# Optimization experiments

Hardware: AMD Instinct MI355X
Metric: run time of the kernel (lower is better)

Reference implementation:

```python
import jax, jax.numpy as jnp
import numpy as np

B, N, E = 256, 128, 262144
LABEL_DIM, MAX_DEGREE, RW_DIM = 29, 16, 16
F = 128
NUM_LABELS = LABEL_DIM + MAX_DEGREE + RW_DIM  # 61
SK_ITER, SK_TAU = 6, 1.0


def _edges(k):
    k1, k2, k3 = jax.random.split(k, 3)
    g = jax.random.randint(k1, (E,), 0, B)
    src = g * N + jax.random.randint(k2, (E,), 0, N)
    dst = g * N + jax.random.randint(k3, (E,), 0, N)
    return src, dst


def setup_inputs():
    key = jax.random.key(0)
    ks = jax.random.split(key, 20)
    ntot = B * N
    s = 0.05
    nrm = lambda k, shp: jax.random.normal(k, shp, dtype=jnp.float32) * s
    src1, dst1 = _edges(ks[3])
    src2, dst2 = _edges(ks[7])
    return {
        'x1': jax.random.uniform(ks[0], (ntot, LABEL_DIM), dtype=jnp.float32),
        'cent1': jax.random.randint(ks[1], (ntot,), 0, MAX_DEGREE),
        'rw1': jax.random.uniform(ks[2], (ntot, RW_DIM), dtype=jnp.float32),
        'src1': src1, 'dst1': dst1,
        'x2': jax.random.uniform(ks[4], (ntot, LABEL_DIM), dtype=jnp.float32),
        'cent2': jax.random.randint(ks[5], (ntot,), 0, MAX_DEGREE),
        'rw2': jax.random.uniform(ks[6], (ntot, RW_DIM), dtype=jnp.float32),
        'src2': src2, 'dst2': dst2,
        'degree_emb': nrm(ks[8], (MAX_DEGREE, MAX_DEGREE)),
        'init_W': nrm(ks[9], (NUM_LABELS, F)), 'init_b': jnp.zeros((F,), jnp.float32),
        'W1': nrm(ks[10], (F, F)), 'b1': jnp.zeros((F,), jnp.float32),
        'W2': nrm(ks[11], (F, F)), 'b2': jnp.zeros((F,), jnp.float32),
        'W3': nrm(ks[12], (F, F)), 'b3': jnp.zeros((F,), jnp.float32),
        'A_aff': nrm(ks[13], (F, F)) + jnp.eye(F, dtype=jnp.float32),
        'sc_W1': nrm(ks[14], (8 * F, 64)), 'sc_b1': jnp.zeros((64,), jnp.float32),
        'sc_W2': nrm(ks[15], (64, 1)), 'sc_b2': jnp.zeros((1,), jnp.float32),
        'topk': 8,
    }


def gcn_conv(x, W, b, src, dst):
    # GCNConv: x' = D^{-1/2} (A + I) D^{-1/2} x W + b
    n = x.shape[0]
    h = x @ W
    loops = jnp.arange(n)
    s = jnp.concatenate([src, loops])
    d = jnp.concatenate([dst, loops])
    deg = jax.ops.segment_sum(jnp.ones_like(d, dtype=h.dtype), d, n)
    dinv = jax.lax.rsqrt(jnp.maximum(deg, 1.0))
    w = dinv[s] * dinv[d]
    return jax.ops.segment_sum(h[s] * w[:, None], d, n) + b


def conv_pass(feat, src, dst, W1, b1, W2, b2, W3, b3):
    f1 = gcn_conv(feat, W1, b1, src, dst)
    f2 = gcn_conv(jax.nn.relu(f1), W2, b2, src, dst)
    f3 = gcn_conv(jax.nn.relu(f2), W3, b3, src, dst)
    return f1, f2, f3


def affinity(xa, xb, A):
    Xa = xa.reshape(B, N, -1)
    Xb = xb.reshape(B, N, -1)
    return jnp.einsum('bif,fg,bjg->bij', Xa, A, Xb)


def soft_topk(scores, ks_tgt, n_iter, tau):
    # Entropic-OT soft top-k (Xie et al.) over flattened affinity entries vs 2 anchors,
    # normalized by SK_ITER log-domain Sinkhorn iterations.
    b, n, m = scores.shape
    L = n * m
    x = scores.reshape(b, L)
    a_lo = x.min(axis=1, keepdims=True) - 1.0
    a_hi = x.max(axis=1, keepdims=True) + 1.0
    anchors = jnp.concatenate([a_lo, a_hi], axis=1)      # [b, 2]
    logK = -jnp.abs(x[:, :, None] - anchors[:, None, :]) / tau  # [b, L, 2]
    log_mu = jnp.full((b, L), -jnp.log(float(L)), dtype=x.dtype)
    k = ks_tgt[:, None]
    nu = jnp.concatenate([(L - k) / L, k / L], axis=1)   # [b, 2]
    log_nu = jnp.log(nu)

    def body(carry, _):
        f, g = carry
        f = log_mu - jax.nn.logsumexp(logK + g[:, None, :], axis=2)
        g = log_nu - jax.nn.logsumexp(logK + f[:, :, None], axis=1)
        return (f, g), None

    init = (jnp.zeros((b, L), x.dtype), jnp.zeros((b, 2), x.dtype))
    (f, g), _ = jax.lax.scan(body, init, None, length=n_iter)
    gamma = jnp.exp(logK + f[:, :, None] + g[:, None, :])
    prob = (gamma[:, :, 1] * L).reshape(b, n, m)
    return gamma, prob


def reference(x1, cent1, rw1, src1, dst1, x2, cent2, rw2, src2, dst2,
              degree_emb, init_W, init_b, W1, b1, W2, b2, W3, b3, A_aff,
              sc_W1, sc_b1, sc_W2, sc_b2, topk):
    feat1 = jax.nn.relu(jnp.concatenate([x1, degree_emb[cent1], rw1], axis=1) @ init_W + init_b)
    feat2 = jax.nn.relu(jnp.concatenate([x2, degree_emb[cent2], rw2], axis=1) @ init_W + init_b)
    f11, f12, f13 = conv_pass(feat1, src1, dst1, W1, b1, W2, b2, W3, b3)
    f21, f22, f23 = conv_pass(feat2, src2, dst2, W1, b1, W2, b2, W3, b3)

    gt_ks = jnp.full((B,), topk / 2.0, dtype=feat1.dtype)
    _, sim1 = soft_topk(affinity(feat1, feat2, A_aff), gt_ks, SK_ITER, SK_TAU)
    _, sim2 = soft_topk(affinity(f13, f23, A_aff), gt_ks, SK_ITER, SK_TAU)

    gf1 = jnp.concatenate([feat1, f11, f12, f13], axis=1).reshape(B, N, -1).sum(axis=1)   # global_add_pool
    gf2 = jnp.concatenate([feat2, f21, f22, f23], axis=1).reshape(B, N, -1).max(axis=1)   # global_max_pool
    scores = jnp.concatenate([gf1, gf2], axis=1)  # [B, 8F]
    h = jax.nn.relu(scores @ sc_W1 + sc_b1)
    ged = jax.nn.sigmoid((h @ sc_W2 + sc_b2).reshape(-1))
    return ged, sim1, sim2
```

## Files before the change

kernel.cpp:

```cpp
#include <hip/hip_runtime.h>
#include <math.h>

#define BATCH 256
#define NNODE 128
#define NT    32768
#define FDIM  128
#define NEDGE 262144
#define LBL   29
#define MAXDEG 16
#define RWD   16
#define NTF   (NT * FDIM)

__global__ void k_deg2(const int* __restrict__ dst1, const int* __restrict__ dst2,
                       int* __restrict__ d1, int* __restrict__ d2) {
  int e = blockIdx.x * 256 + threadIdx.x;
  if (e < NEDGE) atomicAdd(&d1[dst1[e]], 1);
  else if (e < 2 * NEDGE) atomicAdd(&d2[dst2[e - NEDGE]], 1);
}
__global__ __launch_bounds__(1024) void k_scan2(const int* __restrict__ degi1,
                                                int* __restrict__ ofs1, int* __restrict__ cur1,
                                                float* __restrict__ dinv1,
                                                const int* __restrict__ degi2,
                                                int* __restrict__ ofs2, int* __restrict__ cur2,
                                                float* __restrict__ dinv2) {
  const int* degi = blockIdx.x ? degi2 : degi1;
  int* ofs   = blockIdx.x ? ofs2  : ofs1;
  int* cur   = blockIdx.x ? cur2  : cur1;
  float* dnv = blockIdx.x ? dinv2 : dinv1;
  __shared__ int part[1024];
  int t = threadIdx.x;
  int base = t * 32;
  int loc[32]; int sum = 0;
#pragma unroll
  for (int u = 0; u < 32; ++u) {
    int dg = degi[base + u];
    loc[u] = sum; sum += dg;
    dnv[base + u] = rsqrtf((float)(dg + 1));
  }
  part[t] = sum;
  __syncthreads();
  for (int off = 1; off < 1024; off <<= 1) {
    int v = (t >= off) ? part[t - off] : 0;
    __syncthreads();
    part[t] += v;
    __syncthreads();
  }
  int excl = (t == 0) ? 0 : part[t - 1];
#pragma unroll
  for (int u = 0; u < 32; ++u) {
    int o = excl + loc[u];
    ofs[base + u] = o; cur[base + u] = o;
  }
}
__global__ void k_fill2(const int* __restrict__ src1, const int* __restrict__ dst1,
                        int* __restrict__ cur1, int* __restrict__ csr1,
                        const int* __restrict__ src2, const int* __restrict__ dst2,
                        int* __restrict__ cur2, int* __restrict__ csr2) {
  int e = blockIdx.x * 256 + threadIdx.x;
  if (e < NEDGE) {
    int pos = atomicAdd(&cur1[dst1[e]], 1);
    csr1[pos] = src1[e];
  } else if (e < 2 * NEDGE) {
    e -= NEDGE;
    int pos = atomicAdd(&cur2[dst2[e]], 1);
    csr2[pos] = src2[e];
  }
}

__global__ __launch_bounds__(256, 2) void k_chain(
    const float* __restrict__ x1, const int* __restrict__ cent1, const float* __restrict__ rw1,
    const float* __restrict__ x2, const int* __restrict__ cent2, const float* __restrict__ rw2,
    const float* __restrict__ demb,
    const float* __restrict__ initW, const float* __restrict__ initb,
    const float* __restrict__ W1, const float* __restrict__ b1,
    const float* __restrict__ W2, const float* __restrict__ b2,
    const float* __restrict__ W3, const float* __restrict__ b3,
    const int* __restrict__ ofs1, const int* __restrict__ end1, const int* __restrict__ csr1,
    const int* __restrict__ ofs2, const int* __restrict__ end2, const int* __restrict__ csr2,
    const float* __restrict__ dinv1, const float* __restrict__ dinv2,
    float* __restrict__ feat1G, float* __restrict__ feat2G,
    float* __restrict__ f13G, float* __restrict__ f23G,
    float* __restrict__ gfs) {
  __shared__ float X[128 * 132];
  __shared__ float WcB[16 * 132];
  __shared__ float dvL[128];
  __shared__ float bL[128];
  __shared__ int   oL[128], enL[128];

  const int t = threadIdx.x;
  const int side = blockIdx.x >> 8;
  const int g = blockIdx.x & 255;
  const int nb = g * NNODE;

  const float* xg    = side ? x2 : x1;
  const int*   centg = side ? cent2 : cent1;
  const float* rwg   = side ? rw2 : rw1;
  const int*   ofsg  = side ? ofs2 : ofs1;
  const int*   endg  = side ? end2 : end1;
  const int*   csrg  = side ? csr2 : csr1;
  const float* dinvg = side ? dinv2 : dinv1;
  float* featG = side ? feat2G : feat1G;
  float* f3G   = side ? f23G : f13G;

  const int e_base = ofsg[nb];
  if (t < 128) {
    dvL[t] = dinvg[nb + t];
    oL[t]  = ofsg[nb + t] - e_base;
    enL[t] = endg[nb + t] - e_base;
  }
  {
    int d = t >> 1, sub = t & 1;
    int node = nb + d;
    int ct = centg[node];
    const float* xr = xg + (size_t)node * LBL;
    const float* er = demb + ct * MAXDEG;
    const float* rr = rwg + (size_t)node * RWD;
    for (int c = sub * 34; c < sub * 34 + 34; ++c) {
      float v = 0.f;
      if (c < LBL) v = xr[c];
      else if (c < LBL + MAXDEG) v = er[c - LBL];
      else if (c < 61) v = rr[c - 45];
      X[d * 68 + c] = v;
    }
  }
  __syncthreads();

  const int rg = t >> 3;
  const int jq = (t & 7) * 4;

  {
    float acc[4][16] = {};
    for (int kc = 0; kc < 64; kc += 16) {
      __syncthreads();
#pragma unroll
      for (int u = 0; u < 2; ++u) {
        int ll = t + 256 * u;
        int row = ll >> 5, c4 = (ll & 31) * 4;
        int gk = kc + row;
        float4 w = (gk < 61) ? *reinterpret_cast<const float4*>(&initW[(size_t)gk * FDIM + c4])
                             : make_float4(0.f, 0.f, 0.f, 0.f);
        *reinterpret_cast<float4*>(&WcB[row * 132 + c4]) = w;
      }
      if (kc == 0 && t < 128) bL[t] = initb[t];
      __syncthreads();
      for (int kk = 0; kk < 16; kk += 4) {
        float av[4][4];
#pragma unroll
        for (int r = 0; r < 4; ++r) {
          float4 tmp = *reinterpret_cast<const float4*>(&X[(rg + 32 * r) * 68 + kc + kk]);
          av[r][0] = tmp.x; av[r][1] = tmp.y; av[r][2] = tmp.z; av[r][3] = tmp.w;
        }
#pragma unroll
        for (int c = 0; c < 4; ++c) {
          float4 w0 = *reinterpret_cast<const float4*>(&WcB[(kk + c) * 132 + jq]);
          float4 w1 = *reinterpret_cast<const float4*>(&WcB[(kk + c) * 132 + 32 + jq]);
          float4 w2 = *reinterpret_cast<const float4*>(&WcB[(kk + c) * 132 + 64 + jq]);
          float4 w3 = *reinterpret_cast<const float4*>(&WcB[(kk + c) * 132 + 96 + jq]);
#pragma unroll
          for (int r = 0; r < 4; ++r) {
            float a = av[r][c];
            acc[r][0]  += a * w0.x; acc[r][1]  += a * w0.y; acc[r][2]  += a * w0.z; acc[r][3]  += a * w0.w;
            acc[r][4]  += a * w1.x; acc[r][5]  += a * w1.y; acc[r][6]  += a * w1.z; acc[r][7]  += a * w1.w;
            acc[r][8]  += a * w2.x; acc[r][9]  += a * w2.y; acc[r][10] += a * w2.z; acc[r][11] += a * w2.w;
            acc[r][12] += a * w3.x; acc[r][13] += a * w3.y; acc[r][14] += a * w3.z; acc[r][15] += a * w3.w;
          }
        }
      }
    }
    __syncthreads();
#pragma unroll
    for (int r = 0; r < 4; ++r) {
      int row = rg + 32 * r;
#pragma unroll
      for (int q = 0; q < 4; ++q) {
        int col = q * 32 + jq;
        float4 bl = *reinterpret_cast<const float4*>(&bL[col]);
        float4 o = make_float4(fmaxf(acc[r][q * 4 + 0] + bl.x, 0.f),
                               fmaxf(acc[r][q * 4 + 1] + bl.y, 0.f),
                               fmaxf(acc[r][q * 4 + 2] + bl.z, 0.f),
                               fmaxf(acc[r][q * 4 + 3] + bl.w, 0.f));
        *reinterpret_cast<float4*>(&X[row * 132 + col]) = o;
        *reinterpret_cast<float4*>(&featG[(size_t)(nb + row) * FDIM + col]) = o;
      }
    }
    __syncthreads();
  }

#define POOL_LAYER(layer)                                                            \
  {                                                                                  \
    int j4 = (t & 31) * 4, qq = t >> 5;                                              \
    float4 pv = side ? make_float4(-INFINITY, -INFINITY, -INFINITY, -INFINITY)       \
                     : make_float4(0.f, 0.f, 0.f, 0.f);                              \
    for (int r = 0; r < 16; ++r) {                                                   \
      float4 fv = *reinterpret_cast<const float4*>(&X[(qq * 16 + r) * 132 + j4]);    \
      if (side) { pv.x = fmaxf(pv.x, fv.x); pv.y = fmaxf(pv.y, fv.y);                \
                  pv.z = fmaxf(pv.z, fv.z); pv.w = fmaxf(pv.w, fv.w); }              \
      else      { pv.x += fv.x; pv.y += fv.y; pv.z += fv.z; pv.w += fv.w; }          \
    }                                                                                \
    *reinterpret_cast<float4*>(&WcB[qq * 128 + j4]) = pv;                            \
    __syncthreads();                                                                 \
    if (t < 128) {                                                                   \
      float v = side ? -INFINITY : 0.f;                                              \
      for (int q2 = 0; q2 < 8; ++q2) {                                               \
        float w2 = WcB[q2 * 128 + t];                                                \
        v = side ? fmaxf(v, w2) : (v + w2);                                          \
      }                                                                              \
      gfs[g * 1024 + side * 512 + (layer) * 128 + t] = v;                            \
    }                                                                                \
  }

  POOL_LAYER(0)

  for (int l = 0; l < 3; ++l) {
    const float* Wg = (l == 0) ? W1 : (l == 1) ? W2 : W3;
    const float* bg = (l == 0) ? b1 : (l == 1) ? b2 : b3;
    float acc[4][16] = {};
    for (int kc = 0; kc < 128; kc += 16) {
      __syncthreads();
#pragma unroll
      for (int u = 0; u < 2; ++u) {
        int ll = t + 256 * u;
        int row = ll >> 5, c4 = (ll & 31) * 4;
        *reinterpret_cast<float4*>(&WcB[row * 132 + c4]) =
            *reinterpret_cast<const float4*>(&Wg[(size_t)(kc + row) * FDIM + c4]);
      }
      if (kc == 0 && t < 128) bL[t] = bg[t];
      __syncthreads();
      for (int kk = 0; kk < 16; kk += 4) {
        float av[4][4];
#pragma unroll
        for (int r = 0; r < 4; ++r) {
          float4 tmp = *reinterpret_cast<const float4*>(&X[(rg + 32 * r) * 132 + kc + kk]);
          if (l > 0) {
            tmp.x = fmaxf(tmp.x, 0.f); tmp.y = fmaxf(tmp.y, 0.f);
            tmp.z = fmaxf(tmp.z, 0.f); tmp.w = fmaxf(tmp.w, 0.f);
          }
          av[r][0] = tmp.x; av[r][1] = tmp.y; av[r][2] = tmp.z; av[r][3] = tmp.w;
        }
#pragma unroll
        for (int c = 0; c < 4; ++c) {
          float4 w0 = *reinterpret_cast<const float4*>(&WcB[(kk + c) * 132 + jq]);
          float4 w1 = *reinterpret_cast<const float4*>(&WcB[(kk + c) * 132 + 32 + jq]);
          float4 w2 = *reinterpret_cast<const float4*>(&WcB[(kk + c) * 132 + 64 + jq]);
          float4 w3 = *reinterpret_cast<const float4*>(&WcB[(kk + c) * 132 + 96 + jq]);
#pragma unroll
          for (int r = 0; r < 4; ++r) {
            float a = av[r][c];
            acc[r][0]  += a * w0.x; acc[r][1]  += a * w0.y; acc[r][2]  += a * w0.z; acc[r][3]  += a * w0.w;
            acc[r][4]  += a * w1.x; acc[r][5]  += a * w1.y; acc[r][6]  += a * w1.z; acc[r][7]  += a * w1.w;
            acc[r][8]  += a * w2.x; acc[r][9]  += a * w2.y; acc[r][10] += a * w2.z; acc[r][11] += a * w2.w;
            acc[r][12] += a * w3.x; acc[r][13] += a * w3.y; acc[r][14] += a * w3.z; acc[r][15] += a * w3.w;
          }
        }
      }
    }
    __syncthreads();
#pragma unroll
    for (int r = 0; r < 4; ++r) {
      int row = rg + 32 * r;
#pragma unroll
      for (int q = 0; q < 4; ++q) {
        int col = q * 32 + jq;
        *reinterpret_cast<float4*>(&X[row * 132 + col]) =
            make_float4(acc[r][q * 4 + 0], acc[r][q * 4 + 1],
                        acc[r][q * 4 + 2], acc[r][q * 4 + 3]);
      }
    }
    __syncthreads();

    {
      int d = t >> 1, fc = (t & 1) * 64;
      float dd = dvL[d];
      float4 a[16];
#pragma unroll
      for (int u = 0; u < 16; ++u) {
        float4 hv = *reinterpret_cast<const float4*>(&X[d * 132 + fc + u * 4]);
        a[u] = make_float4(dd * hv.x, dd * hv.y, dd * hv.z, dd * hv.w);
      }
      int o0 = oL[d], o1 = enL[d];
      int sj = (o0 < o1) ? (csrg[e_base + o0] - nb) : 0;
      for (int j = o0; j < o1; ++j) {
        int sn = (j + 1 < o1) ? (csrg[e_base + j + 1] - nb) : 0;
        float w = dvL[sj];
#pragma unroll
        for (int u = 0; u < 16; ++u) {
          float4 hv = *reinterpret_cast<const float4*>(&X[sj * 132 + fc + u * 4]);
          a[u].x += w * hv.x; a[u].y += w * hv.y; a[u].z += w * hv.z; a[u].w += w * hv.w;
        }
        sj = sn;
      }
      __syncthreads();
#pragma unroll
      for (int u = 0; u < 16; ++u) {
        float4 bl = *reinterpret_cast<const float4*>(&bL[fc + u * 4]);
        float4 o = make_float4(bl.x + dd * a[u].x, bl.y + dd * a[u].y,
                               bl.z + dd * a[u].z, bl.w + dd * a[u].w);
        *reinterpret_cast<float4*>(&X[d * 132 + fc + u * 4]) = o;
        if (l == 2)
          *reinterpret_cast<float4*>(&f3G[(size_t)(nb + d) * FDIM + fc + u * 4]) = o;
      }
    }
    __syncthreads();

    POOL_LAYER(l + 1)
  }
#undef POOL_LAYER
}

__global__ __launch_bounds__(1024) void k_sim(const float* __restrict__ F1s1,
                                              const float* __restrict__ F2s1,
                                              const float* __restrict__ F1s2,
                                              const float* __restrict__ F2s2,
                                              const float* __restrict__ Aaff,
                                              const int* __restrict__ topk,
                                              float* __restrict__ S1,
                                              float* __restrict__ S2) {
  __shared__ float X1[128 * 132];
  __shared__ float X2[128 * 132];
  __shared__ float rA[16], rB[16], bc[2];

  const int t = threadIdx.x;
  const int half = blockIdx.x >> 8;
  const int b = blockIdx.x & 255;
  const float* F1b = (half ? F1s2 : F1s1) + (size_t)b * NNODE * FDIM;
  const float* F2b = (half ? F2s2 : F2s1) + (size_t)b * NNODE * FDIM;
  float* Sout = (half ? S2 : S1) + (size_t)b * NNODE * NNODE;

#pragma unroll
  for (int p = 0; p < 4; ++p) {
    int fi = t + 1024 * p;
    int row = fi >> 5, c4 = (fi & 31) * 4;
    *reinterpret_cast<float4*>(&X1[row * 132 + c4]) =
        *reinterpret_cast<const float4*>(&Aaff[(size_t)row * FDIM + c4]);
  }
  {
    int row = t >> 3;
    int cq  = (t & 7) * 4;
#pragma unroll
    for (int p = 0; p < 4; ++p) {
      int c4 = p * 32 + cq;
      float4 v = *reinterpret_cast<const float4*>(&F2b[(size_t)row * FDIM + c4]);
      X2[(c4 + 0) * 132 + row] = v.x;
      X2[(c4 + 1) * 132 + row] = v.y;
      X2[(c4 + 2) * 132 + row] = v.z;
      X2[(c4 + 3) * 132 + row] = v.w;
    }
  }
  __syncthreads();

  const int rg = t >> 3;
  const int jq = (t & 7) * 4;
  const float* f1row = F1b + (size_t)rg * FDIM;

  float acc[16];
#pragma unroll
  for (int u = 0; u < 16; ++u) acc[u] = 0.f;

  for (int k0 = 0; k0 < 128; k0 += 4) {
    float4 a4 = *reinterpret_cast<const float4*>(&f1row[k0]);
    float av[4] = {a4.x, a4.y, a4.z, a4.w};
#pragma unroll
    for (int c = 0; c < 4; ++c) {
      const float* wb = &X1[(k0 + c) * 132];
      float4 w0 = *reinterpret_cast<const float4*>(&wb[jq]);
      float4 w1 = *reinterpret_cast<const float4*>(&wb[32 + jq]);
      float4 w2 = *reinterpret_cast<const float4*>(&wb[64 + jq]);
      float4 w3 = *reinterpret_cast<const float4*>(&wb[96 + jq]);
      float a = av[c];
      acc[0]  += a * w0.x; acc[1]  += a * w0.y; acc[2]  += a * w0.z; acc[3]  += a * w0.w;
      acc[4]  += a * w1.x; acc[5]  += a * w1.y; acc[6]  += a * w1.z; acc[7]  += a * w1.w;
      acc[8]  += a * w2.x; acc[9]  += a * w2.y; acc[10] += a * w2.z; acc[11] += a * w2.w;
      acc[12] += a * w3.x; acc[13] += a * w3.y; acc[14] += a * w3.z; acc[15] += a * w3.w;
    }
  }
  __syncthreads();
#pragma unroll
  for (int q = 0; q < 4; ++q)
    *reinterpret_cast<float4*>(&X1[rg * 132 + 32 * q + jq]) =
        make_float4(acc[q * 4 + 0], acc[q * 4 + 1], acc[q * 4 + 2], acc[q * 4 + 3]);

#pragma unroll
  for (int u = 0; u < 16; ++u) acc[u] = 0.f;
  __syncthreads();

  for (int k0 = 0; k0 < 128; k0 += 4) {
    float4 a4 = *reinterpret_cast<const float4*>(&X1[rg * 132 + k0]);
    float av[4] = {a4.x, a4.y, a4.z, a4.w};
#pragma unroll
    for (int c = 0; c < 4; ++c) {
      const float* wb = &X2[(k0 + c) * 132];
      float4 w0 = *reinterpret_cast<const float4*>(&wb[jq]);
      float4 w1 = *reinterpret_cast<const float4*>(&wb[32 + jq]);
      float4 w2 = *reinterpret_cast<const float4*>(&wb[64 + jq]);
      float4 w3 = *reinterpret_cast<const float4*>(&wb[96 + jq]);
      float a = av[c];
      acc[0]  += a * w0.x; acc[1]  += a * w0.y; acc[2]  += a * w0.z; acc[3]  += a * w0.w;
      acc[4]  += a * w1.x; acc[5]  += a * w1.y; acc[6]  += a * w1.z; acc[7]  += a * w1.w;
      acc[8]  += a * w2.x; acc[9]  += a * w2.y; acc[10] += a * w2.z; acc[11] += a * w2.w;
      acc[12] += a * w3.x; acc[13] += a * w3.y; acc[14] += a * w3.z; acc[15] += a * w3.w;
    }
  }

  const int wave = t >> 6, lane = t & 63;
  {
    float mn = acc[0], mx = acc[0];
#pragma unroll
    for (int u = 1; u < 16; ++u) { mn = fminf(mn, acc[u]); mx = fmaxf(mx, acc[u]); }
    for (int off = 32; off; off >>= 1) {
      mn = fminf(mn, __shfl_down(mn, off));
      mx = fmaxf(mx, __shfl_down(mx, off));
    }
    if (lane == 0) { rA[wave] = mn; rB[wave] = mx; }
    __syncthreads();
    if (t < 16) {
      mn = rA[t]; mx = rB[t];
      for (int off = 8; off; off >>= 1) {
        mn = fminf(mn, __shfl_down(mn, off));
        mx = fmaxf(mx, __shfl_down(mx, off));
      }
      if (t == 0) { bc[0] = mn - 1.f; bc[1] = mx + 1.f; }
    }
    __syncthreads();
  }
  float a_lo = bc[0], a_hi = bc[1];

  float p[16], q[16];
#pragma unroll
  for (int u = 0; u < 16; ++u) {
    p[u] = __expf(a_lo - acc[u]);
    q[u] = __expf(acc[u] - a_hi);
  }

  const float Lf = (float)(NNODE * NNODE);
  float kt = 0.5f * (float)topk[0];

  float E0 = 1.f, E1 = 1.f, E0p = 1.f, E1p = 1.f;
  for (int it = 0; it < 6; ++it) {
    E0p = E0; E1p = E1;
    float r0 = 0.f, r1 = 0.f;
#pragma unroll
    for (int u = 0; u < 16; ++u) {
      float denom = fmaf(p[u], E0, q[u] * E1);
      float rin = __builtin_amdgcn_rcpf(denom);
      r0 = fmaf(p[u], rin, r0);
      r1 = fmaf(q[u], rin, r1);
    }
    for (int off = 32; off; off >>= 1) {
      r0 += __shfl_down(r0, off);
      r1 += __shfl_down(r1, off);
    }
    if (lane == 0) { rA[wave] = r0; rB[wave] = r1; }
    __syncthreads();
    if (t < 16) {
      r0 = rA[t]; r1 = rB[t];
      for (int off = 8; off; off >>= 1) {
        r0 += __shfl_down(r0, off);
        r1 += __shfl_down(r1, off);
      }
      if (t == 0) { bc[0] = (Lf - kt) / r0; bc[1] = kt / r1; }
    }
    __syncthreads();
    E0 = bc[0]; E1 = bc[1];
    __syncthreads();
  }

  float* xrow = Sout + (size_t)rg * NNODE;
#pragma unroll
  for (int qd = 0; qd < 4; ++qd) {
    float o[4];
#pragma unroll
    for (int j = 0; j < 4; ++j) {
      int u = qd * 4 + j;
      float denom = fmaf(p[u], E0p, q[u] * E1p);
      o[j] = q[u] * E1 * __builtin_amdgcn_rcpf(denom);
    }
    *reinterpret_cast<float4*>(&xrow[32 * qd + jq]) = make_float4(o[0], o[1], o[2], o[3]);
  }
}

__global__ __launch_bounds__(256) void k_mlp(const float* __restrict__ gfs,
                                             const float* __restrict__ W1,
                                             const float* __restrict__ b1,
                                             const float* __restrict__ W2,
                                             const float* __restrict__ b2,
                                             float* __restrict__ ged) {
  __shared__ float sm[1024];
  int b = blockIdx.x, t = threadIdx.x;
  const float* s = gfs + b * 1024;
#pragma unroll
  for (int qq = 0; qq < 4; ++qq) sm[t + 256 * qq] = s[t + 256 * qq];
  __syncthreads();
  int j4 = (t & 15) * 4, kp = t >> 4;
  float4 acc = make_float4(0.f, 0.f, 0.f, 0.f);
#pragma unroll 8
  for (int k = 0; k < 64; ++k) {
    float4 w = *reinterpret_cast<const float4*>(&W1[(size_t)(kp * 64 + k) * 64 + j4]);
    float sv = sm[kp * 64 + k];
    acc.x += sv * w.x; acc.y += sv * w.y; acc.z += sv * w.z; acc.w += sv * w.w;
  }
  __syncthreads();
  *reinterpret_cast<float4*>(&sm[kp * 64 + j4]) = acc;
  __syncthreads();
  if (t < 64) {
    float h = b1[t];
#pragma unroll
    for (int kp2 = 0; kp2 < 16; ++kp2) h += sm[kp2 * 64 + t];
    h = fmaxf(h, 0.f);
    float v = h * W2[t];
    for (int off = 32; off; off >>= 1) v += __shfl_down(v, off);
    if (t == 0) ged[b] = 1.f / (1.f + __expf(-(v + b2[0])));
  }
}

extern "C" void kernel_launch(void* const* d_in, const int* in_sizes, int n_in,
                              void* d_out, int out_size, void* d_ws, size_t ws_size,
                              hipStream_t stream) {
  (void)in_sizes; (void)n_in; (void)out_size; (void)ws_size;
  const float* x1    = (const float*)d_in[0];
  const int*   cent1 = (const int*)  d_in[1];
  const float* rw1   = (const float*)d_in[2];
  const int*   src1  = (const int*)  d_in[3];
  const int*   dst1  = (const int*)  d_in[4];
  const float* x2    = (const float*)d_in[5];
  const int*   cent2 = (const int*)  d_in[6];
  const float* rw2   = (const float*)d_in[7];
  const int*   src2  = (const int*)  d_in[8];
  const int*   dst2  = (const int*)  d_in[9];
  const float* demb  = (const float*)d_in[10];
  const float* initW = (const float*)d_in[11];
  const float* initb = (const float*)d_in[12];
  const float* W1    = (const float*)d_in[13];
  const float* b1    = (const float*)d_in[14];
  const float* W2    = (const float*)d_in[15];
  const float* b2    = (const float*)d_in[16];
  const float* W3    = (const float*)d_in[17];
  const float* b3    = (const float*)d_in[18];
  const float* Aaff  = (const float*)d_in[19];
  const float* scW1  = (const float*)d_in[20];
  const float* scb1  = (const float*)d_in[21];
  const float* scW2  = (const float*)d_in[22];
  const float* scb2  = (const float*)d_in[23];
  const int*   topk  = (const int*)  d_in[24];

  float* ws    = (float*)d_ws;
  float* feat1 = ws;
  float* feat2 = ws + (size_t)1 * NTF;
  float* f13   = ws + (size_t)2 * NTF;
  float* f23   = ws + (size_t)3 * NTF;
  float* dinv1 = ws + (size_t)4 * NTF;
  float* dinv2 = dinv1 + NT;
  float* gfs   = dinv2 + NT;

  float* ged = (float*)d_out;
  float* S1  = ged + BATCH;
  float* S2  = S1 + (size_t)BATCH * NNODE * NNODE;

  int* degi1 = (int*)S1;
  int* ofs1  = degi1 + NT;
  int* cur1  = ofs1 + NT;
  int* csr1  = cur1 + NT;
  int* degi2 = csr1 + NEDGE;
  int* ofs2  = degi2 + NT;
  int* cur2  = ofs2 + NT;
  int* csr2  = cur2 + NT;

  const int gE = NEDGE / 256;

  hipMemsetAsync(degi1, 0, NT * sizeof(int), stream);
  hipMemsetAsync(degi2, 0, NT * sizeof(int), stream);
  k_deg2<<<2 * gE, 256, 0, stream>>>(dst1, dst2, degi1, degi2);
  k_scan2<<<2, 1024, 0, stream>>>(degi1, ofs1, cur1, dinv1, degi2, ofs2, cur2, dinv2);
  k_fill2<<<2 * gE, 256, 0, stream>>>(src1, dst1, cur1, csr1, src2, dst2, cur2, csr2);

  k_chain<<<512, 256, 0, stream>>>(
      x1, cent1, rw1, x2, cent2, rw2, demb, initW, initb,
      W1, b1, W2, b2, W3, b3,
      ofs1, cur1, csr1, ofs2, cur2, csr2, dinv1, dinv2,
      feat1, feat2, f13, f23, gfs);

  k_mlp<<<BATCH, 256, 0, stream>>>(gfs, scW1, scb1, scW2, scb2, ged);

  k_sim<<<512, 1024, 0, stream>>>(feat1, feat2, f13, f23, Aaff, topk, S1, S2);
}
```

Before: 442.8 us.

## Use per-graph CSR scan with fixed edge stride; read GEMM weights from global

The CSR offset scan now runs as 512 small blocks, one per graph and side, using wavefront shuffles. Each graph gets a fixed 2048-slot edge region, replacing the two 1024-thread blocks that each scanned 32768 nodes serially. Separately, the three GCN layer GEMMs now read weight rows straight from global memory (relying on the cache) instead of staging 16-row tiles in LDS, which removes two barriers per k-chunk. The fixed stride assumes no graph has more than 2048 incoming edges. Reading weights from global could add latency in the inner FMA loop.

Result: slower. 709.4 us (+60.2%).

```diff
diff --git a/kernel.cpp b/kernel.cpp
--- a/kernel.cpp
+++ b/kernel.cpp
@@ -10,6 +10,7 @@
 #define MAXDEG 16
 #define RWD   16
 #define NTF   (NT * FDIM)
+#define ESTRIDE 2048
 
 __global__ void k_deg2(const int* __restrict__ dst1, const int* __restrict__ dst2,
                        int* __restrict__ d1, int* __restrict__ d2) {
@@ -17,40 +18,35 @@
   if (e < NEDGE) atomicAdd(&d1[dst1[e]], 1);
   else if (e < 2 * NEDGE) atomicAdd(&d2[dst2[e - NEDGE]], 1);
 }
-__global__ __launch_bounds__(1024) void k_scan2(const int* __restrict__ degi1,
-                                                int* __restrict__ ofs1, int* __restrict__ cur1,
-                                                float* __restrict__ dinv1,
-                                                const int* __restrict__ degi2,
-                                                int* __restrict__ ofs2, int* __restrict__ cur2,
-                                                float* __restrict__ dinv2) {
-  const int* degi = blockIdx.x ? degi2 : degi1;
-  int* ofs   = blockIdx.x ? ofs2  : ofs1;
-  int* cur   = blockIdx.x ? cur2  : cur1;
-  float* dnv = blockIdx.x ? dinv2 : dinv1;
-  __shared__ int part[1024];
-  int t = threadIdx.x;
-  int base = t * 32;
-  int loc[32]; int sum = 0;
-#pragma unroll
-  for (int u = 0; u < 32; ++u) {
-    int dg = degi[base + u];
-    loc[u] = sum; sum += dg;
-    dnv[base + u] = rsqrtf((float)(dg + 1));
-  }
-  part[t] = sum;
-  __syncthreads();
-  for (int off = 1; off < 1024; off <<= 1) {
-    int v = (t >= off) ? part[t - off] : 0;
-    __syncthreads();
-    part[t] += v;
-    __syncthreads();
-  }
-  int excl = (t == 0) ? 0 : part[t - 1];
-#pragma unroll
-  for (int u = 0; u < 32; ++u) {
-    int o = excl + loc[u];
-    ofs[base + u] = o; cur[base + u] = o;
-  }
+__global__ __launch_bounds__(128) void k_scanl(const int* __restrict__ degi1,
+                                               int* __restrict__ ofs1, int* __restrict__ cur1,
+                                               float* __restrict__ dinv1,
+                                               const int* __restrict__ degi2,
+                                               int* __restrict__ ofs2, int* __restrict__ cur2,
+                                               float* __restrict__ dinv2) {
+  const int side = blockIdx.x >> 8;
+  const int g = blockIdx.x & 255;
+  const int* degi = side ? degi2 : degi1;
+  int* ofs   = side ? ofs2  : ofs1;
+  int* cur   = side ? cur2  : cur1;
+  float* dnv = side ? dinv2 : dinv1;
+  const int t = threadIdx.x;
+  const int node = g * NNODE + t;
+  int dg = degi[node];
+  dnv[node] = rsqrtf((float)(dg + 1));
+  int lane = t & 63, wv = t >> 6;
+  int v = dg;
+  for (int off = 1; off < 64; off <<= 1) {
+    int u = __shfl_up(v, off);
+    if (lane >= off) v += u;
+  }
+  __shared__ int wsum[2];
+  if (lane == 63) wsum[wv] = v;
+  __syncthreads();
+  int excl = v - dg + (wv ? wsum[0] : 0);
+  int base = g * ESTRIDE + excl;
+  ofs[node] = base;
+  cur[node] = base;
 }
 __global__ void k_fill2(const int* __restrict__ src1, const int* __restrict__ dst1,
                         int* __restrict__ cur1, int* __restrict__ csr1,
@@ -214,43 +210,34 @@
   for (int l = 0; l < 3; ++l) {
     const float* Wg = (l == 0) ? W1 : (l == 1) ? W2 : W3;
     const float* bg = (l == 0) ? b1 : (l == 1) ? b2 : b3;
+    if (t < 128) bL[t] = bg[t];
     float acc[4][16] = {};
-    for (int kc = 0; kc < 128; kc += 16) {
-      __syncthreads();
-#pragma unroll
-      for (int u = 0; u < 2; ++u) {
-        int ll = t + 256 * u;
-        int row = ll >> 5, c4 = (ll & 31) * 4;
-        *reinterpret_cast<float4*>(&WcB[row * 132 + c4]) =
-            *reinterpret_cast<const float4*>(&Wg[(size_t)(kc + row) * FDIM + c4]);
-      }
-      if (kc == 0 && t < 128) bL[t] = bg[t];
-      __syncthreads();
-      for (int kk = 0; kk < 16; kk += 4) {
-        float av[4][4];
+#pragma unroll 4
+    for (int k0 = 0; k0 < 128; k0 += 4) {
+      float av[4][4];
+#pragma unroll
+      for (int r = 0; r < 4; ++r) {
+        float4 tmp = *reinterpret_cast<const float4*>(&X[(rg + 32 * r) * 132 + k0]);
+        if (l > 0) {
+          tmp.x = fmaxf(tmp.x, 0.f); tmp.y = fmaxf(tmp.y, 0.f);
+          tmp.z = fmaxf(tmp.z, 0.f); tmp.w = fmaxf(tmp.w, 0.f);
+        }
+        av[r][0] = tmp.x; av[r][1] = tmp.y; av[r][2] = tmp.z; av[r][3] = tmp.w;
+      }
+#pragma unroll
+      for (int c = 0; c < 4; ++c) {
+        const float* wr = Wg + (size_t)(k0 + c) * FDIM;
+        float4 w0 = *reinterpret_cast<const float4*>(&wr[jq]);
+        float4 w1 = *reinterpret_cast<const float4*>(&wr[32 + jq]);
+        float4 w2 = *reinterpret_cast<const float4*>(&wr[64 + jq]);
+        float4 w3 = *reinterpret_cast<const float4*>(&wr[96 + jq]);
 #pragma unroll
         for (int r = 0; r < 4; ++r) {
-          float4 tmp = *reinterpret_cast<const float4*>(&X[(rg + 32 * r) * 132 + kc + kk]);
-          if (l > 0) {
-            tmp.x = fmaxf(tmp.x, 0.f); tmp.y = fmaxf(tmp.y, 0.f);
-            tmp.z = fmaxf(tmp.z, 0.f); tmp.w = fmaxf(tmp.w, 0.f);
-          }
-          av[r][0] = tmp.x; av[r][1] = tmp.y; av[r][2] = tmp.z; av[r][3] = tmp.w;
-        }
-#pragma unroll
-        for (int c = 0; c < 4; ++c) {
-          float4 w0 = *reinterpret_cast<const float4*>(&WcB[(kk + c) * 132 + jq]);
-          float4 w1 = *reinterpret_cast<const float4*>(&WcB[(kk + c) * 132 + 32 + jq]);
-          float4 w2 = *reinterpret_cast<const float4*>(&WcB[(kk + c) * 132 + 64 + jq]);
-          float4 w3 = *reinterpret_cast<const float4*>(&WcB[(kk + c) * 132 + 96 + jq]);
-#pragma unroll
-          for (int r = 0; r < 4; ++r) {
-            float a = av[r][c];
-            acc[r][0]  += a * w0.x; acc[r][1]  += a * w0.y; acc[r][2]  += a * w0.z; acc[r][3]  += a * w0.w;
-            acc[r][4]  += a * w1.x; acc[r][5]  += a * w1.y; acc[r][6]  += a * w1.z; acc[r][7]  += a * w1.w;
-            acc[r][8]  += a * w2.x; acc[r][9]  += a * w2.y; acc[r][10] += a * w2.z; acc[r][11] += a * w2.w;
-            acc[r][12] += a * w3.x; acc[r][13] += a * w3.y; acc[r][14] += a * w3.z; acc[r][15] += a * w3.w;
-          }
+          float a = av[r][c];
+          acc[r][0]  += a * w0.x; acc[r][1]  += a * w0.y; acc[r][2]  += a * w0.z; acc[r][3]  += a * w0.w;
+          acc[r][4]  += a * w1.x; acc[r][5]  += a * w1.y; acc[r][6]  += a * w1.z; acc[r][7]  += a * w1.w;
+          acc[r][8]  += a * w2.x; acc[r][9]  += a * w2.y; acc[r][10] += a * w2.z; acc[r][11] += a * w2.w;
+          acc[r][12] += a * w3.x; acc[r][13] += a * w3.y; acc[r][14] += a * w3.z; acc[r][15] += a * w3.w;
         }
       }
     }
@@ -559,7 +546,7 @@
   int* ofs1  = degi1 + NT;
   int* cur1  = ofs1 + NT;
   int* csr1  = cur1 + NT;
-  int* degi2 = csr1 + NEDGE;
+  int* degi2 = csr1 + BATCH * ESTRIDE;
   int* ofs2  = degi2 + NT;
   int* cur2  = ofs2 + NT;
   int* csr2  = cur2 + NT;
@@ -569,7 +556,7 @@
   hipMemsetAsync(degi1, 0, NT * sizeof(int), stream);
   hipMemsetAsync(degi2, 0, NT * sizeof(int), stream);
   k_deg2<<<2 * gE, 256, 0, stream>>>(dst1, dst2, degi1, degi2);
-  k_scan2<<<2, 1024, 0, stream>>>(degi1, ofs1, cur1, dinv1, degi2, ofs2, cur2, dinv2);
+  k_scanl<<<512, 128, 0, stream>>>(degi1, ofs1, cur1, dinv1, degi2, ofs2, cur2, dinv2);
   k_fill2<<<2 * gE, 256, 0, stream>>>(src1, dst1, cur1, csr1, src2, dst2, cur2, csr2);
 
   k_chain<<<512, 256, 0, stream>>>(
```
